# Kernel optimization log

Measured on AMD Instinct MI355X. Metric: run time of the kernel, lower is better.

Reference implementation:

```python
import jax, jax.numpy as jnp
import numpy as np

BITS = 4
GROUP_SIZE = 128
VALS_PER_I32 = 32 // BITS  # 8
MASK = (1 << BITS) - 1     # 15


def setup_inputs() -> dict:
    key = jax.random.key(0)
    k1, k2, k3, k4, k5 = jax.random.split(key, 5)
    M, K, N = 8, 4096, 14336
    packed_K = K // VALS_PER_I32          # 512
    num_groups = K // GROUP_SIZE          # 32
    x = jax.random.normal(k1, (M, K), dtype=jnp.float16)
    qweight = jax.random.randint(k2, (N, packed_K), 0, 2147483647, dtype=jnp.int32)
    scale = jax.random.uniform(k3, (N, num_groups), dtype=jnp.float16) * jnp.float16(0.02)
    zero_point = jax.random.uniform(k4, (N, num_groups), dtype=jnp.float16) * jnp.float16(MASK)
    bias = jax.random.normal(k5, (N,), dtype=jnp.float16)
    return {"x": x, "qweight": qweight, "scale": scale, "zero_point": zero_point, "bias": bias}


def _dequantize(qweight, scale, zero_point):
    # qweight: [N, packed_K] int32; scale/zp: [N, num_groups]
    N, packed_K = qweight.shape
    K = packed_K * VALS_PER_I32
    shifts = (jnp.arange(VALS_PER_I32, dtype=jnp.int32) * BITS)  # [8]
    # unpack: low nibble first, matching (packed >> (idx_in_packed*bits)) & mask
    q = (qweight[:, :, None] >> shifts[None, None, :]) & MASK    # [N, packed_K, 8]
    q = q.reshape(N, K // GROUP_SIZE, GROUP_SIZE)                # [N, G, gs]
    s = scale.astype(jnp.float32)[:, :, None]
    z = zero_point.astype(jnp.float32)[:, :, None]
    w = s * (q.astype(jnp.float32) - z)                          # fp32 dequant as in kernel
    return w.reshape(N, K).astype(jnp.float16)


def reference(x, qweight, scale, zero_point, bias):
    # x: [..., K] -> reshape to [M, K] in fp16 (matches x_reshaped.to(float16))
    orig_shape = x.shape
    xr = x.reshape(-1, orig_shape[-1]).astype(jnp.float16)
    w = _dequantize(qweight, scale, zero_point)                  # [N, K] fp16
    c = xr @ w.T                                                 # [M, N]
    c = c + bias
    return c.reshape(*orig_shape[:-1], w.shape[0])
```

## Files before the change

### kernel.cpp

```cpp
#include <hip/hip_runtime.h>
#include <hip/hip_bf16.h>

#define KDIM 4096
#define PACKED_K 512
#define NGROUPS 32

typedef __bf16 bf16x8 __attribute__((ext_vector_type(8)));
typedef float  f32x4  __attribute__((ext_vector_type(4)));

__device__ __forceinline__ bool detect_f32(const void* sc) {
    const int lane = threadIdx.x & 63;
    const unsigned w = reinterpret_cast<const unsigned*>(sc)[lane];
    const unsigned eb = (w >> 7) & 0xFFu;
    const unsigned long long m = __ballot(eb >= 96u && eb <= 127u);
    return __popcll(m) < 40;
}

template<bool IS_F32, int SPLITK>
__device__ __forceinline__ void qlin_body(
    const void* __restrict__ xv,
    const int*  __restrict__ qw,
    const void* __restrict__ scv,
    const void* __restrict__ zpv,
    const void* __restrict__ biasv,
    float*      __restrict__ ws,
    void*       __restrict__ outv,
    int M, int N)
{
    const int lane = threadIdx.x & 63;
    const int widx = threadIdx.x >> 6;
    const int col  = lane & 15;
    const int c4   = lane >> 4;

    int ntile, ks;
    if (SPLITK == 4) { ntile = blockIdx.x;            ks = widx; }
    else             { ntile = blockIdx.x * 4 + widx; ks = 0;    }
    if (ntile >= (N >> 4)) return;

    const int n = (ntile << 4) + col;
    const int nrounds = NGROUPS / SPLITK;
    const int wbase   = ks * nrounds * 16;

    f32x4 acc = {0.f, 0.f, 0.f, 0.f};
    const int arow = col;

    for (int r = 0; r < nrounds; ++r) {
        const int wb = wbase + r * 16;
        const int g  = wb >> 4;

        float sf, zf;
        if (IS_F32) {
            sf = reinterpret_cast<const float*>(scv)[n * NGROUPS + g];
            zf = reinterpret_cast<const float*>(zpv)[n * NGROUPS + g];
        } else {
            sf = __bfloat162float(reinterpret_cast<const __hip_bfloat16*>(scv)[n * NGROUPS + g]);
            zf = __bfloat162float(reinterpret_cast<const __hip_bfloat16*>(zpv)[n * NGROUPS + g]);
        }
        const float nsz = -sf * zf;

        const int4 w4 = *reinterpret_cast<const int4*>(&qw[(size_t)n * PACKED_K + wb + c4 * 4]);
        const unsigned uw[4] = {(unsigned)w4.x, (unsigned)w4.y, (unsigned)w4.z, (unsigned)w4.w};

#pragma unroll
        for (int t = 0; t < 4; ++t) {
            const int kw = wb + c4 * 4 + t;

            const unsigned u = uw[t];
            union { bf16x8 v; __hip_bfloat16 h[8]; } bfrag;
#pragma unroll
            for (int j = 0; j < 8; ++j)
                bfrag.h[j] = __float2bfloat16(fmaf((float)((u >> (4 * j)) & 15u), sf, nsz));

            union { bf16x8 v; __hip_bfloat16 h[8]; } afrag;
            if (arow < M) {
                if (IS_F32) {
                    const float* xf = reinterpret_cast<const float*>(xv) + (size_t)arow * KDIM + (size_t)kw * 8;
                    const float4 xa = *reinterpret_cast<const float4*>(xf);
                    const float4 xb = *reinterpret_cast<const float4*>(xf + 4);
                    afrag.h[0] = __float2bfloat16(xa.x); afrag.h[1] = __float2bfloat16(xa.y);
                    afrag.h[2] = __float2bfloat16(xa.z); afrag.h[3] = __float2bfloat16(xa.w);
                    afrag.h[4] = __float2bfloat16(xb.x); afrag.h[5] = __float2bfloat16(xb.y);
                    afrag.h[6] = __float2bfloat16(xb.z); afrag.h[7] = __float2bfloat16(xb.w);
                } else {
                    afrag.v = *reinterpret_cast<const bf16x8*>(
                        reinterpret_cast<const __hip_bfloat16*>(xv) + (size_t)arow * KDIM + (size_t)kw * 8);
                }
            } else {
                afrag.v = (bf16x8){};
            }

            acc = __builtin_amdgcn_mfma_f32_16x16x32_bf16(afrag.v, bfrag.v, acc, 0, 0, 0);
        }
    }

    const int rbase = c4 * 4;
    if (SPLITK == 4) {
#pragma unroll
        for (int i = 0; i < 4; ++i) {
            const int row = rbase + i;
            if (row < M) atomicAdd(&ws[(size_t)row * N + n], acc[i]);
        }
    } else {
        float bf;
        if (IS_F32) bf = reinterpret_cast<const float*>(biasv)[n];
        else        bf = __bfloat162float(reinterpret_cast<const __hip_bfloat16*>(biasv)[n]);
#pragma unroll
        for (int i = 0; i < 4; ++i) {
            const int row = rbase + i;
            if (row < M) {
                const float v = acc[i] + bf;
                if (IS_F32) reinterpret_cast<float*>(outv)[(size_t)row * N + n] = v;
                else reinterpret_cast<__hip_bfloat16*>(outv)[(size_t)row * N + n] = __float2bfloat16(v);
            }
        }
    }
}

template<int SPLITK>
__global__ __launch_bounds__(256) void qlin_mfma(
    const void* x, const int* qw, const void* sc, const void* zp,
    const void* bias, float* ws, void* out, int M, int N)
{
    if (detect_f32(sc)) qlin_body<true,  SPLITK>(x, qw, sc, zp, bias, ws, out, M, N);
    else                qlin_body<false, SPLITK>(x, qw, sc, zp, bias, ws, out, M, N);
}

__global__ __launch_bounds__(256) void qlin_epilogue(
    const float* __restrict__ ws, const void* __restrict__ sc,
    const void* __restrict__ biasv, void* __restrict__ outv, int M, int N)
{
    const bool isf = detect_f32(sc);
    const int i = blockIdx.x * 256 + threadIdx.x;
    if (i < M * N) {
        const int nn = i % N;
        const float b = isf ? reinterpret_cast<const float*>(biasv)[nn]
                            : __bfloat162float(reinterpret_cast<const __hip_bfloat16*>(biasv)[nn]);
        const float v = ws[i] + b;
        if (isf) reinterpret_cast<float*>(outv)[i] = v;
        else     reinterpret_cast<__hip_bfloat16*>(outv)[i] = __float2bfloat16(v);
    }
}

extern "C" void kernel_launch(void* const* d_in, const int* in_sizes, int n_in,
                              void* d_out, int out_size, void* d_ws, size_t ws_size,
                              hipStream_t stream)
{
    const void* x    = d_in[0];
    const int*  qw   = (const int*)d_in[1];
    const void* sc   = d_in[2];
    const void* zp   = d_in[3];
    const void* bias = d_in[4];

    const int N = in_sizes[4];
    const int M = in_sizes[0] / KDIM;
    const int ntiles = N >> 4;

    const size_t need = (size_t)M * N * sizeof(float);
    if (ws_size >= need) {
        hipMemsetAsync(d_ws, 0, need, stream);
        qlin_mfma<4><<<ntiles, 256, 0, stream>>>(x, qw, sc, zp, bias, (float*)d_ws, d_out, M, N);
        const int total = M * N;
        qlin_epilogue<<<(total + 255) / 256, 256, 0, stream>>>((const float*)d_ws, sc, bias, d_out, M, N);
    } else {
        qlin_mfma<1><<<(ntiles + 3) / 4, 256, 0, stream>>>(x, qw, sc, zp, bias, nullptr, d_out, M, N);
    }
}
```

Before: 43.33 us.

## Split K into 8 slices with batched upfront loads per wave

The main kernel now splits K into 8 slices across two blocks per N tile, so each wave handles 4 groups. Each wave issues all of its weight, scale/zero and activation loads up front before the dequant and MFMA loop, which exposes more memory-level parallelism. The change also doubles the grid, vectorizes the scale/zero loads, clamps activation rows so x is never read out of bounds, and skips atomics for the padded rows 8-15. In exchange it uses more registers and doubles the number of atomic adds into the workspace.

Result: no change. 43.26 us (-0.2%).

```diff
diff --git a/kernel.cpp b/kernel.cpp
--- a/kernel.cpp
+++ b/kernel.cpp
@@ -1,135 +1,145 @@
 #include <hip/hip_runtime.h>
 #include <hip/hip_bf16.h>
 
-#define KDIM 4096
+#define KDIM     4096
 #define PACKED_K 512
-#define NGROUPS 32
+#define NGROUPS  32
+#define GPW      4
+#define NSLICES  8
 
 typedef __bf16 bf16x8 __attribute__((ext_vector_type(8)));
 typedef float  f32x4  __attribute__((ext_vector_type(4)));
+
+union ABu { bf16x8 v; __hip_bfloat16 h[8]; unsigned d[4]; };
 
 __device__ __forceinline__ bool detect_f32(const void* sc) {
     const int lane = threadIdx.x & 63;
     const unsigned w = reinterpret_cast<const unsigned*>(sc)[lane];
     const unsigned eb = (w >> 7) & 0xFFu;
-    const unsigned long long m = __ballot(eb >= 96u && eb <= 127u);
-    return __popcll(m) < 40;
-}
-
-template<bool IS_F32, int SPLITK>
-__device__ __forceinline__ void qlin_body(
-    const void* __restrict__ xv,
-    const int*  __restrict__ qw,
-    const void* __restrict__ scv,
-    const void* __restrict__ zpv,
-    const void* __restrict__ biasv,
-    float*      __restrict__ ws,
-    void*       __restrict__ outv,
-    int M, int N)
-{
-    const int lane = threadIdx.x & 63;
-    const int widx = threadIdx.x >> 6;
-    const int col  = lane & 15;
-    const int c4   = lane >> 4;
-
-    int ntile, ks;
-    if (SPLITK == 4) { ntile = blockIdx.x;            ks = widx; }
-    else             { ntile = blockIdx.x * 4 + widx; ks = 0;    }
-    if (ntile >= (N >> 4)) return;
-
+    return __popcll(__ballot(eb >= 96u && eb <= 127u)) < 40;
+}
+
+template<bool IS_F32>
+__device__ __forceinline__ f32x4 slice_acc(
+    const void* __restrict__ xv, const int* __restrict__ qw,
+    const void* __restrict__ scv, const void* __restrict__ zpv,
+    int n, int arow, int c4, int kslice)
+{
+    const int gbase = kslice * GPW;
+    const int wb0   = gbase << 4;
+
+    const int* qbase = qw + (size_t)n * PACKED_K + wb0 + (c4 << 2);
+    int4 q[GPW];
+#pragma unroll
+    for (int r = 0; r < GPW; ++r)
+        q[r] = *reinterpret_cast<const int4*>(qbase + (r << 4));
+
+    float s[GPW], z[GPW];
+    if (IS_F32) {
+        const float4 sv = *reinterpret_cast<const float4*>(
+            reinterpret_cast<const float*>(scv) + (size_t)n * NGROUPS + gbase);
+        const float4 zv = *reinterpret_cast<const float4*>(
+            reinterpret_cast<const float*>(zpv) + (size_t)n * NGROUPS + gbase);
+        s[0]=sv.x; s[1]=sv.y; s[2]=sv.z; s[3]=sv.w;
+        z[0]=zv.x; z[1]=zv.y; z[2]=zv.z; z[3]=zv.w;
+    } else {
+        const ushort4 sv = *reinterpret_cast<const ushort4*>(
+            reinterpret_cast<const unsigned short*>(scv) + (size_t)n * NGROUPS + gbase);
+        const ushort4 zv = *reinterpret_cast<const ushort4*>(
+            reinterpret_cast<const unsigned short*>(zpv) + (size_t)n * NGROUPS + gbase);
+        const unsigned short se[4] = {sv.x, sv.y, sv.z, sv.w};
+        const unsigned short ze[4] = {zv.x, zv.y, zv.z, zv.w};
+#pragma unroll
+        for (int r = 0; r < GPW; ++r) {
+            union { unsigned u; float f; } cs, cz;
+            cs.u = (unsigned)se[r] << 16; cz.u = (unsigned)ze[r] << 16;
+            s[r] = cs.f; z[r] = cz.f;
+        }
+    }
+
+    ABu a[GPW][4];
+    if (IS_F32) {
+        const float* xb = reinterpret_cast<const float*>(xv) + (size_t)arow * KDIM;
+#pragma unroll
+        for (int r = 0; r < GPW; ++r)
+#pragma unroll
+        for (int t = 0; t < 4; ++t) {
+            const int kw = wb0 + (r << 4) + (c4 << 2) + t;
+            const float4 xa = *reinterpret_cast<const float4*>(xb + (size_t)kw * 8);
+            const float4 xc = *reinterpret_cast<const float4*>(xb + (size_t)kw * 8 + 4);
+            a[r][t].h[0] = __float2bfloat16(xa.x); a[r][t].h[1] = __float2bfloat16(xa.y);
+            a[r][t].h[2] = __float2bfloat16(xa.z); a[r][t].h[3] = __float2bfloat16(xa.w);
+            a[r][t].h[4] = __float2bfloat16(xc.x); a[r][t].h[5] = __float2bfloat16(xc.y);
+            a[r][t].h[6] = __float2bfloat16(xc.z); a[r][t].h[7] = __float2bfloat16(xc.w);
+        }
+    } else {
+        const __hip_bfloat16* xb = reinterpret_cast<const __hip_bfloat16*>(xv) + (size_t)arow * KDIM;
+#pragma unroll
+        for (int r = 0; r < GPW; ++r)
+#pragma unroll
+        for (int t = 0; t < 4; ++t) {
+            const int kw = wb0 + (r << 4) + (c4 << 2) + t;
+            a[r][t].v = *reinterpret_cast<const bf16x8*>(xb + (size_t)kw * 8);
+        }
+    }
+
+    f32x4 acc = {0.f, 0.f, 0.f, 0.f};
+#pragma unroll
+    for (int r = 0; r < GPW; ++r) {
+        const float sf = s[r];
+        const float nsz = -s[r] * z[r];
+        const unsigned uw[4] = {(unsigned)q[r].x, (unsigned)q[r].y, (unsigned)q[r].z, (unsigned)q[r].w};
+#pragma unroll
+        for (int t = 0; t < 4; ++t) {
+            ABu b;
+#pragma unroll
+            for (int j = 0; j < 8; ++j)
+                b.h[j] = __float2bfloat16(fmaf((float)((uw[t] >> (4 * j)) & 15u), sf, nsz));
+            acc = __builtin_amdgcn_mfma_f32_16x16x32_bf16(a[r][t].v, b.v, acc, 0, 0, 0);
+        }
+    }
+    return acc;
+}
+
+template<bool IS_F32>
+__device__ __forceinline__ void main_body(
+    const void* xv, const int* qw, const void* scv, const void* zpv,
+    float* ws, int M, int N)
+{
+    const int lane  = threadIdx.x & 63;
+    const int widx  = threadIdx.x >> 6;
+    const int col   = lane & 15;
+    const int c4    = lane >> 4;
+    const int ntile  = blockIdx.x >> 1;
+    const int kslice = ((blockIdx.x & 1) << 2) | widx;
     const int n = (ntile << 4) + col;
-    const int nrounds = NGROUPS / SPLITK;
-    const int wbase   = ks * nrounds * 16;
-
-    f32x4 acc = {0.f, 0.f, 0.f, 0.f};
-    const int arow = col;
-
-    for (int r = 0; r < nrounds; ++r) {
-        const int wb = wbase + r * 16;
-        const int g  = wb >> 4;
-
-        float sf, zf;
-        if (IS_F32) {
-            sf = reinterpret_cast<const float*>(scv)[n * NGROUPS + g];
-            zf = reinterpret_cast<const float*>(zpv)[n * NGROUPS + g];
-        } else {
-            sf = __bfloat162float(reinterpret_cast<const __hip_bfloat16*>(scv)[n * NGROUPS + g]);
-            zf = __bfloat162float(reinterpret_cast<const __hip_bfloat16*>(zpv)[n * NGROUPS + g]);
-        }
-        const float nsz = -sf * zf;
-
-        const int4 w4 = *reinterpret_cast<const int4*>(&qw[(size_t)n * PACKED_K + wb + c4 * 4]);
-        const unsigned uw[4] = {(unsigned)w4.x, (unsigned)w4.y, (unsigned)w4.z, (unsigned)w4.w};
-
-#pragma unroll
-        for (int t = 0; t < 4; ++t) {
-            const int kw = wb + c4 * 4 + t;
-
-            const unsigned u = uw[t];
-            union { bf16x8 v; __hip_bfloat16 h[8]; } bfrag;
-#pragma unroll
-            for (int j = 0; j < 8; ++j)
-                bfrag.h[j] = __float2bfloat16(fmaf((float)((u >> (4 * j)) & 15u), sf, nsz));
-
-            union { bf16x8 v; __hip_bfloat16 h[8]; } afrag;
-            if (arow < M) {
-                if (IS_F32) {
-                    const float* xf = reinterpret_cast<const float*>(xv) + (size_t)arow * KDIM + (size_t)kw * 8;
-                    const float4 xa = *reinterpret_cast<const float4*>(xf);
-                    const float4 xb = *reinterpret_cast<const float4*>(xf + 4);
-                    afrag.h[0] = __float2bfloat16(xa.x); afrag.h[1] = __float2bfloat16(xa.y);
-                    afrag.h[2] = __float2bfloat16(xa.z); afrag.h[3] = __float2bfloat16(xa.w);
-                    afrag.h[4] = __float2bfloat16(xb.x); afrag.h[5] = __float2bfloat16(xb.y);
-                    afrag.h[6] = __float2bfloat16(xb.z); afrag.h[7] = __float2bfloat16(xb.w);
-                } else {
-                    afrag.v = *reinterpret_cast<const bf16x8*>(
-                        reinterpret_cast<const __hip_bfloat16*>(xv) + (size_t)arow * KDIM + (size_t)kw * 8);
-                }
-            } else {
-                afrag.v = (bf16x8){};
-            }
-
-            acc = __builtin_amdgcn_mfma_f32_16x16x32_bf16(afrag.v, bfrag.v, acc, 0, 0, 0);
-        }
-    }
-
-    const int rbase = c4 * 4;
-    if (SPLITK == 4) {
+    int arow = col & 7;
+    if (arow >= M) arow = M - 1;
+
+    const f32x4 acc = slice_acc<IS_F32>(xv, qw, scv, zpv, n, arow, c4, kslice);
+
+    if (c4 < 2) {
 #pragma unroll
         for (int i = 0; i < 4; ++i) {
-            const int row = rbase + i;
+            const int row = (c4 << 2) + i;
             if (row < M) atomicAdd(&ws[(size_t)row * N + n], acc[i]);
         }
-    } else {
-        float bf;
-        if (IS_F32) bf = reinterpret_cast<const float*>(biasv)[n];
-        else        bf = __bfloat162float(reinterpret_cast<const __hip_bfloat16*>(biasv)[n]);
-#pragma unroll
-        for (int i = 0; i < 4; ++i) {
-            const int row = rbase + i;
-            if (row < M) {
-                const float v = acc[i] + bf;
-                if (IS_F32) reinterpret_cast<float*>(outv)[(size_t)row * N + n] = v;
-                else reinterpret_cast<__hip_bfloat16*>(outv)[(size_t)row * N + n] = __float2bfloat16(v);
-            }
-        }
-    }
-}
-
-template<int SPLITK>
-__global__ __launch_bounds__(256) void qlin_mfma(
-    const void* x, const int* qw, const void* sc, const void* zp,
-    const void* bias, float* ws, void* out, int M, int N)
-{
-    if (detect_f32(sc)) qlin_body<true,  SPLITK>(x, qw, sc, zp, bias, ws, out, M, N);
-    else                qlin_body<false, SPLITK>(x, qw, sc, zp, bias, ws, out, M, N);
+    }
+}
+
+__global__ __launch_bounds__(256, 4) void qlin_main(
+    const void* xv, const int* __restrict__ qw, const void* scv, const void* zpv,
+    float* __restrict__ ws, int M, int N)
+{
+    if (detect_f32(scv)) main_body<true >(xv, qw, scv, zpv, ws, M, N);
+    else                 main_body<false>(xv, qw, scv, zpv, ws, M, N);
 }
 
 __global__ __launch_bounds__(256) void qlin_epilogue(
-    const float* __restrict__ ws, const void* __restrict__ sc,
+    const float* __restrict__ ws, const void* __restrict__ scv,
     const void* __restrict__ biasv, void* __restrict__ outv, int M, int N)
 {
-    const bool isf = detect_f32(sc);
+    const bool isf = detect_f32(scv);
     const int i = blockIdx.x * 256 + threadIdx.x;
     if (i < M * N) {
         const int nn = i % N;
@@ -141,6 +151,51 @@
     }
 }
 
+template<bool IS_F32>
+__device__ __forceinline__ void fb_body(
+    const void* xv, const int* qw, const void* scv, const void* zpv,
+    const void* biasv, void* outv, int M, int N)
+{
+    const int lane = threadIdx.x & 63;
+    const int widx = threadIdx.x >> 6;
+    const int col  = lane & 15;
+    const int c4   = lane >> 4;
+    const int ntile = blockIdx.x * 4 + widx;
+    if (ntile >= (N >> 4)) return;
+    const int n = (ntile << 4) + col;
+    int arow = col & 7;
+    if (arow >= M) arow = M - 1;
+
+    f32x4 acc = {0.f, 0.f, 0.f, 0.f};
+#pragma unroll 1
+    for (int ks = 0; ks < NSLICES; ++ks) {
+        const f32x4 p = slice_acc<IS_F32>(xv, qw, scv, zpv, n, arow, c4, ks);
+        acc[0] += p[0]; acc[1] += p[1]; acc[2] += p[2]; acc[3] += p[3];
+    }
+    if (c4 < 2) {
+        float b;
+        if (IS_F32) b = reinterpret_cast<const float*>(biasv)[n];
+        else        b = __bfloat162float(reinterpret_cast<const __hip_bfloat16*>(biasv)[n]);
+#pragma unroll
+        for (int i = 0; i < 4; ++i) {
+            const int row = (c4 << 2) + i;
+            if (row < M) {
+                const float v = acc[i] + b;
+                if (IS_F32) reinterpret_cast<float*>(outv)[(size_t)row * N + n] = v;
+                else reinterpret_cast<__hip_bfloat16*>(outv)[(size_t)row * N + n] = __float2bfloat16(v);
+            }
+        }
+    }
+}
+
+__global__ __launch_bounds__(256) void qlin_fallback(
+    const void* xv, const int* __restrict__ qw, const void* scv, const void* zpv,
+    const void* biasv, void* outv, int M, int N)
+{
+    if (detect_f32(scv)) fb_body<true >(xv, qw, scv, zpv, biasv, outv, M, N);
+    else                 fb_body<false>(xv, qw, scv, zpv, biasv, outv, M, N);
+}
+
 extern "C" void kernel_launch(void* const* d_in, const int* in_sizes, int n_in,
                               void* d_out, int out_size, void* d_ws, size_t ws_size,
                               hipStream_t stream)
@@ -158,10 +213,10 @@
     const size_t need = (size_t)M * N * sizeof(float);
     if (ws_size >= need) {
         hipMemsetAsync(d_ws, 0, need, stream);
-        qlin_mfma<4><<<ntiles, 256, 0, stream>>>(x, qw, sc, zp, bias, (float*)d_ws, d_out, M, N);
+        qlin_main<<<ntiles * 2, 256, 0, stream>>>(x, qw, sc, zp, (float*)d_ws, M, N);
         const int total = M * N;
         qlin_epilogue<<<(total + 255) / 256, 256, 0, stream>>>((const float*)d_ws, sc, bias, d_out, M, N);
     } else {
-        qlin_mfma<1><<<(ntiles + 3) / 4, 256, 0, stream>>>(x, qw, sc, zp, bias, nullptr, d_out, M, N);
-    }
-}
+        qlin_fallback<<<(ntiles + 3) / 4, 256, 0, stream>>>(x, qw, sc, zp, bias, d_out, M, N);
+    }
+}
```

## Fuse split-K reduction into one kernel with LDS reduce and prefetch

Applied to the files above, without the earlier changes.

Drops the workspace memset, the atomicAdd split-K and the separate epilogue kernel. The four waves of a block now each cover 8 groups, and their partial sums are combined through shared memory before the bias add and the store, all in one launch. It also loads all scale and zero-point values up front with vector loads, double-buffers the weight and activation loads across groups, and sets launch bounds for occupancy. The cost is more registers and one block-wide barrier.

New measurement: 40.22 us. 1.08x faster.

```diff
diff --git a/kernel.cpp b/kernel.cpp
--- a/kernel.cpp
+++ b/kernel.cpp
@@ -1,144 +1,168 @@
 #include <hip/hip_runtime.h>
 #include <hip/hip_bf16.h>
 
-#define KDIM 4096
+#define KDIM     4096
 #define PACKED_K 512
-#define NGROUPS 32
+#define NGROUPS  32
+#define GPWAVE   8
 
 typedef __bf16 bf16x8 __attribute__((ext_vector_type(8)));
 typedef float  f32x4  __attribute__((ext_vector_type(4)));
+
+union ABu { bf16x8 v; __hip_bfloat16 h[8]; unsigned d[4]; };
 
 __device__ __forceinline__ bool detect_f32(const void* sc) {
     const int lane = threadIdx.x & 63;
     const unsigned w = reinterpret_cast<const unsigned*>(sc)[lane];
     const unsigned eb = (w >> 7) & 0xFFu;
-    const unsigned long long m = __ballot(eb >= 96u && eb <= 127u);
-    return __popcll(m) < 40;
+    return __popcll(__ballot(eb >= 96u && eb <= 127u)) < 40;
 }
 
-template<bool IS_F32, int SPLITK>
-__device__ __forceinline__ void qlin_body(
+template<bool IS_F32>
+__device__ __forceinline__ void fused_body(
     const void* __restrict__ xv,
     const int*  __restrict__ qw,
     const void* __restrict__ scv,
     const void* __restrict__ zpv,
     const void* __restrict__ biasv,
-    float*      __restrict__ ws,
     void*       __restrict__ outv,
-    int M, int N)
+    int M, int N, float* __restrict__ red)
 {
     const int lane = threadIdx.x & 63;
     const int widx = threadIdx.x >> 6;
     const int col  = lane & 15;
     const int c4   = lane >> 4;
+    const int n    = (blockIdx.x << 4) + col;
+    int arow = col & 7;
+    if (arow >= M) arow = M - 1;
 
-    int ntile, ks;
-    if (SPLITK == 4) { ntile = blockIdx.x;            ks = widx; }
-    else             { ntile = blockIdx.x * 4 + widx; ks = 0;    }
-    if (ntile >= (N >> 4)) return;
+    const int g0 = widx * GPWAVE;
 
-    const int n = (ntile << 4) + col;
-    const int nrounds = NGROUPS / SPLITK;
-    const int wbase   = ks * nrounds * 16;
-
-    f32x4 acc = {0.f, 0.f, 0.f, 0.f};
-    const int arow = col;
-
-    for (int r = 0; r < nrounds; ++r) {
-        const int wb = wbase + r * 16;
-        const int g  = wb >> 4;
-
-        float sf, zf;
-        if (IS_F32) {
-            sf = reinterpret_cast<const float*>(scv)[n * NGROUPS + g];
-            zf = reinterpret_cast<const float*>(zpv)[n * NGROUPS + g];
-        } else {
-            sf = __bfloat162float(reinterpret_cast<const __hip_bfloat16*>(scv)[n * NGROUPS + g]);
-            zf = __bfloat162float(reinterpret_cast<const __hip_bfloat16*>(zpv)[n * NGROUPS + g]);
-        }
-        const float nsz = -sf * zf;
-
-        const int4 w4 = *reinterpret_cast<const int4*>(&qw[(size_t)n * PACKED_K + wb + c4 * 4]);
-        const unsigned uw[4] = {(unsigned)w4.x, (unsigned)w4.y, (unsigned)w4.z, (unsigned)w4.w};
-
+    float s[GPWAVE], z[GPWAVE];
+    if (IS_F32) {
+        const float* sp = reinterpret_cast<const float*>(scv) + (size_t)n * NGROUPS + g0;
+        const float* zp = reinterpret_cast<const float*>(zpv) + (size_t)n * NGROUPS + g0;
+        const float4 s0 = *reinterpret_cast<const float4*>(sp);
+        const float4 s1 = *reinterpret_cast<const float4*>(sp + 4);
+        const float4 z0 = *reinterpret_cast<const float4*>(zp);
+        const float4 z1 = *reinterpret_cast<const float4*>(zp + 4);
+        s[0]=s0.x; s[1]=s0.y; s[2]=s0.z; s[3]=s0.w; s[4]=s1.x; s[5]=s1.y; s[6]=s1.z; s[7]=s1.w;
+        z[0]=z0.x; z[1]=z0.y; z[2]=z0.z; z[3]=z0.w; z[4]=z1.x; z[5]=z1.y; z[6]=z1.z; z[7]=z1.w;
+    } else {
+        const unsigned short* sp = reinterpret_cast<const unsigned short*>(scv) + (size_t)n * NGROUPS + g0;
+        const unsigned short* zp = reinterpret_cast<const unsigned short*>(zpv) + (size_t)n * NGROUPS + g0;
+        const ushort4 s0 = *reinterpret_cast<const ushort4*>(sp);
+        const ushort4 s1 = *reinterpret_cast<const ushort4*>(sp + 4);
+        const ushort4 z0 = *reinterpret_cast<const ushort4*>(zp);
+        const ushort4 z1 = *reinterpret_cast<const ushort4*>(zp + 4);
+        const unsigned short se[8] = {s0.x,s0.y,s0.z,s0.w,s1.x,s1.y,s1.z,s1.w};
+        const unsigned short ze[8] = {z0.x,z0.y,z0.z,z0.w,z1.x,z1.y,z1.z,z1.w};
 #pragma unroll
-        for (int t = 0; t < 4; ++t) {
-            const int kw = wb + c4 * 4 + t;
-
-            const unsigned u = uw[t];
-            union { bf16x8 v; __hip_bfloat16 h[8]; } bfrag;
-#pragma unroll
-            for (int j = 0; j < 8; ++j)
-                bfrag.h[j] = __float2bfloat16(fmaf((float)((u >> (4 * j)) & 15u), sf, nsz));
-
-            union { bf16x8 v; __hip_bfloat16 h[8]; } afrag;
-            if (arow < M) {
-                if (IS_F32) {
-                    const float* xf = reinterpret_cast<const float*>(xv) + (size_t)arow * KDIM + (size_t)kw * 8;
-                    const float4 xa = *reinterpret_cast<const float4*>(xf);
-                    const float4 xb = *reinterpret_cast<const float4*>(xf + 4);
-                    afrag.h[0] = __float2bfloat16(xa.x); afrag.h[1] = __float2bfloat16(xa.y);
-                    afrag.h[2] = __float2bfloat16(xa.z); afrag.h[3] = __float2bfloat16(xa.w);
-                    afrag.h[4] = __float2bfloat16(xb.x); afrag.h[5] = __float2bfloat16(xb.y);
-                    afrag.h[6] = __float2bfloat16(xb.z); afrag.h[7] = __float2bfloat16(xb.w);
-                } else {
-                    afrag.v = *reinterpret_cast<const bf16x8*>(
-                        reinterpret_cast<const __hip_bfloat16*>(xv) + (size_t)arow * KDIM + (size_t)kw * 8);
-                }
-            } else {
-                afrag.v = (bf16x8){};
-            }
-
-            acc = __builtin_amdgcn_mfma_f32_16x16x32_bf16(afrag.v, bfrag.v, acc, 0, 0, 0);
+        for (int r = 0; r < GPWAVE; ++r) {
+            union { unsigned u; float f; } cs, cz;
+            cs.u = (unsigned)se[r] << 16; cz.u = (unsigned)ze[r] << 16;
+            s[r] = cs.f; z[r] = cz.f;
         }
     }
 
-    const int rbase = c4 * 4;
-    if (SPLITK == 4) {
+    const int* qbase = qw + (size_t)n * PACKED_K + (g0 << 4) + (c4 << 2);
+    const float* xf = IS_F32 ? reinterpret_cast<const float*>(xv) + (size_t)arow * KDIM : nullptr;
+    const __hip_bfloat16* xh = IS_F32 ? nullptr
+        : reinterpret_cast<const __hip_bfloat16*>(xv) + (size_t)arow * KDIM;
+
+    int4   qb[2];
+    float4 xb[2][4][2];
+    bf16x8 xb16[2][4];
+
+    {
+        const int kw0 = (g0 << 4) + (c4 << 2);
+        qb[0] = *reinterpret_cast<const int4*>(qbase);
 #pragma unroll
-        for (int i = 0; i < 4; ++i) {
-            const int row = rbase + i;
-            if (row < M) atomicAdd(&ws[(size_t)row * N + n], acc[i]);
-        }
-    } else {
-        float bf;
-        if (IS_F32) bf = reinterpret_cast<const float*>(biasv)[n];
-        else        bf = __bfloat162float(reinterpret_cast<const __hip_bfloat16*>(biasv)[n]);
-#pragma unroll
-        for (int i = 0; i < 4; ++i) {
-            const int row = rbase + i;
-            if (row < M) {
-                const float v = acc[i] + bf;
-                if (IS_F32) reinterpret_cast<float*>(outv)[(size_t)row * N + n] = v;
-                else reinterpret_cast<__hip_bfloat16*>(outv)[(size_t)row * N + n] = __float2bfloat16(v);
+        for (int t = 0; t < 4; ++t) {
+            if (IS_F32) {
+                xb[0][t][0] = *reinterpret_cast<const float4*>(xf + (size_t)(kw0 + t) * 8);
+                xb[0][t][1] = *reinterpret_cast<const float4*>(xf + (size_t)(kw0 + t) * 8 + 4);
+            } else {
+                xb16[0][t] = *reinterpret_cast<const bf16x8*>(xh + (size_t)(kw0 + t) * 8);
             }
         }
     }
+
+    f32x4 acc = {0.f, 0.f, 0.f, 0.f};
+
+#pragma unroll
+    for (int r = 0; r < GPWAVE; ++r) {
+        const int cur = r & 1, nxt = cur ^ 1;
+        if (r + 1 < GPWAVE) {
+            const int kw1 = ((g0 + r + 1) << 4) + (c4 << 2);
+            qb[nxt] = *reinterpret_cast<const int4*>(qbase + ((r + 1) << 4));
+#pragma unroll
+            for (int t = 0; t < 4; ++t) {
+                if (IS_F32) {
+                    xb[nxt][t][0] = *reinterpret_cast<const float4*>(xf + (size_t)(kw1 + t) * 8);
+                    xb[nxt][t][1] = *reinterpret_cast<const float4*>(xf + (size_t)(kw1 + t) * 8 + 4);
+                } else {
+                    xb16[nxt][t] = *reinterpret_cast<const bf16x8*>(xh + (size_t)(kw1 + t) * 8);
+                }
+            }
+        }
+
+        const float sf  = s[r];
+        const float nsz = -s[r] * z[r];
+        const unsigned uw[4] = {(unsigned)qb[cur].x, (unsigned)qb[cur].y,
+                                (unsigned)qb[cur].z, (unsigned)qb[cur].w};
+#pragma unroll
+        for (int t = 0; t < 4; ++t) {
+            ABu b;
+#pragma unroll
+            for (int j = 0; j < 8; ++j)
+                b.h[j] = __float2bfloat16(fmaf((float)((uw[t] >> (4 * j)) & 15u), sf, nsz));
+
+            ABu a;
+            if (IS_F32) {
+                const float4 xa = xb[cur][t][0], xc = xb[cur][t][1];
+                a.h[0] = __float2bfloat16(xa.x); a.h[1] = __float2bfloat16(xa.y);
+                a.h[2] = __float2bfloat16(xa.z); a.h[3] = __float2bfloat16(xa.w);
+                a.h[4] = __float2bfloat16(xc.x); a.h[5] = __float2bfloat16(xc.y);
+                a.h[6] = __float2bfloat16(xc.z); a.h[7] = __float2bfloat16(xc.w);
+            } else {
+                a.v = xb16[cur][t];
+            }
+            acc = __builtin_amdgcn_mfma_f32_16x16x32_bf16(a.v, b.v, acc, 0, 0, 0);
+        }
+    }
+
+    float* myred = red + ((size_t)(widx * 64 + lane) << 2);
+    myred[0] = acc[0]; myred[1] = acc[1]; myred[2] = acc[2]; myred[3] = acc[3];
+    __syncthreads();
+
+    const int tid = threadIdx.x;
+    const int row = tid >> 4;
+    const int cc  = tid & 15;
+    if (row < M) {
+        const int lsrc = ((row >> 2) << 4) | cc;
+        const int reg  = row & 3;
+        const float v0 = red[((0 * 64 + lsrc) << 2) + reg];
+        const float v1 = red[((1 * 64 + lsrc) << 2) + reg];
+        const float v2 = red[((2 * 64 + lsrc) << 2) + reg];
+        const float v3 = red[((3 * 64 + lsrc) << 2) + reg];
+        const int nn = (blockIdx.x << 4) + cc;
+        float bsum;
+        if (IS_F32) bsum = reinterpret_cast<const float*>(biasv)[nn];
+        else        bsum = __bfloat162float(reinterpret_cast<const __hip_bfloat16*>(biasv)[nn]);
+        const float v = (v0 + v1) + (v2 + v3) + bsum;
+        if (IS_F32) reinterpret_cast<float*>(outv)[(size_t)row * N + nn] = v;
+        else reinterpret_cast<__hip_bfloat16*>(outv)[(size_t)row * N + nn] = __float2bfloat16(v);
+    }
 }
 
-template<int SPLITK>
-__global__ __launch_bounds__(256) void qlin_mfma(
-    const void* x, const int* qw, const void* sc, const void* zp,
-    const void* bias, float* ws, void* out, int M, int N)
+__global__ __launch_bounds__(256, 3) void qlin_fused(
+    const void* xv, const int* __restrict__ qw, const void* scv, const void* zpv,
+    const void* biasv, void* outv, int M, int N)
 {
-    if (detect_f32(sc)) qlin_body<true,  SPLITK>(x, qw, sc, zp, bias, ws, out, M, N);
-    else                qlin_body<false, SPLITK>(x, qw, sc, zp, bias, ws, out, M, N);
-}
-
-__global__ __launch_bounds__(256) void qlin_epilogue(
-    const float* __restrict__ ws, const void* __restrict__ sc,
-    const void* __restrict__ biasv, void* __restrict__ outv, int M, int N)
-{
-    const bool isf = detect_f32(sc);
-    const int i = blockIdx.x * 256 + threadIdx.x;
-    if (i < M * N) {
-        const int nn = i % N;
-        const float b = isf ? reinterpret_cast<const float*>(biasv)[nn]
-                            : __bfloat162float(reinterpret_cast<const __hip_bfloat16*>(biasv)[nn]);
-        const float v = ws[i] + b;
-        if (isf) reinterpret_cast<float*>(outv)[i] = v;
-        else     reinterpret_cast<__hip_bfloat16*>(outv)[i] = __float2bfloat16(v);
-    }
+    __shared__ float red[4 * 64 * 4];
+    if (detect_f32(scv)) fused_body<true >(xv, qw, scv, zpv, biasv, outv, M, N, red);
+    else                 fused_body<false>(xv, qw, scv, zpv, biasv, outv, M, N, red);
 }
 
 extern "C" void kernel_launch(void* const* d_in, const int* in_sizes, int n_in,
@@ -155,13 +179,5 @@
     const int M = in_sizes[0] / KDIM;
     const int ntiles = N >> 4;
 
-    const size_t need = (size_t)M * N * sizeof(float);
-    if (ws_size >= need) {
-        hipMemsetAsync(d_ws, 0, need, stream);
-        qlin_mfma<4><<<ntiles, 256, 0, stream>>>(x, qw, sc, zp, bias, (float*)d_ws, d_out, M, N);
-        const int total = M * N;
-        qlin_epilogue<<<(total + 255) / 256, 256, 0, stream>>>((const float*)d_ws, sc, bias, d_out, M, N);
-    } else {
-        qlin_mfma<1><<<(ntiles + 3) / 4, 256, 0, stream>>>(x, qw, sc, zp, bias, nullptr, d_out, M, N);
-    }
+    qlin_fused<<<ntiles, 256, 0, stream>>>(x, qw, sc, zp, bias, d_out, M, N);
 }
```
